# Kernel optimization log

Hardware: AMD Instinct MI355X
Metric: run time of the kernel (lower is better)

## Reference

```python
import jax, jax.numpy as jnp
import numpy as np

B, T, D, H = 2, 2048, 1024, 16
HD = D // H  # head_dim = 64


def apply_rope(x, cos, sin):
    # x: [B, H, T, HD]; cos/sin: [1, 1, T, HD//2]
    x1, x2 = x[..., ::2], x[..., 1::2]
    y1 = x1 * cos - x2 * sin
    y2 = x1 * sin + x2 * cos
    # interleave back: [..., HD//2, 2] -> [..., HD]
    return jnp.stack([y1, y2], axis=-1).reshape(x.shape)


def setup_inputs() -> dict:
    key = jax.random.key(0)
    ks = jax.random.split(key, 11)
    s = 0.02
    return {
        "x": jax.random.normal(ks[0], (B, T, D), jnp.float32),
        "cos": jax.random.normal(ks[1], (1, 1, T, HD // 2), jnp.float32),
        "sin": jax.random.normal(ks[2], (1, 1, T, HD // 2), jnp.float32),
        "Wq": jax.random.normal(ks[3], (D, D), jnp.float32) * s,
        "bq": jax.random.normal(ks[4], (D,), jnp.float32) * s,
        "Wk": jax.random.normal(ks[5], (D, D), jnp.float32) * s,
        "bk": jax.random.normal(ks[6], (D,), jnp.float32) * s,
        "Wv": jax.random.normal(ks[7], (D, D), jnp.float32) * s,
        "bv": jax.random.normal(ks[8], (D,), jnp.float32) * s,
        "Wo": jax.random.normal(ks[9], (D, D), jnp.float32) * s,
        "bo": jax.random.normal(ks[10], (D,), jnp.float32) * s,
    }


def reference(x, cos, sin, Wq, bq, Wk, bk, Wv, bv, Wo, bo):
    b, t, d = x.shape
    # projections (nn.Linear: x @ W.T + b)
    q = (x @ Wq.T + bq).reshape(b, t, H, HD).transpose(0, 2, 1, 3)
    k = (x @ Wk.T + bk).reshape(b, t, H, HD).transpose(0, 2, 1, 3)
    v = (x @ Wv.T + bv).reshape(b, t, H, HD).transpose(0, 2, 1, 3)
    q = apply_rope(q, cos, sin)
    k = apply_rope(k, cos, sin)
    scores = jnp.einsum("bhqd,bhkd->bhqk", q, k) / jnp.sqrt(jnp.asarray(HD, x.dtype))
    # causal mask: query i attends to keys j <= i
    causal = jnp.tril(jnp.ones((t, t), dtype=bool))
    scores = jnp.where(causal, scores, jnp.asarray(-jnp.inf, x.dtype))
    weights = jax.nn.softmax(scores, axis=-1)
    out = jnp.einsum("bhqk,bhkd->bhqd", weights, v)
    out = out.transpose(0, 2, 1, 3).reshape(b, t, d)
    return out @ Wo.T + bo
```

## Files before the change

### kernel.cpp

```cpp
#include <hip/hip_runtime.h>
#include <hip/hip_bf16.h>
#include <cstdint>
#include <cstddef>

typedef __attribute__((ext_vector_type(8))) short bf16x8;
typedef __attribute__((ext_vector_type(4))) float f32x4;
typedef __attribute__((ext_vector_type(16))) float f32x16;

#define SCALE2 0.180336880111112f
#define VSTRIDE 2080

__device__ __forceinline__ unsigned short f2bf(float f) {
    unsigned u = __builtin_bit_cast(unsigned, f);
    unsigned r = (u + 0x7FFFu + ((u >> 16) & 1u)) >> 16;
    return (unsigned short)r;
}

__device__ __forceinline__ void gload16(const unsigned short* g, unsigned short* l) {
    __builtin_amdgcn_global_load_lds(
        (const __attribute__((address_space(1))) unsigned int*)(g),
        (__attribute__((address_space(3))) unsigned int*)(l), 16, 0, 0);
}

__global__ void cvt_all(const float* __restrict__ x,
                        const float* __restrict__ wq, const float* __restrict__ wk,
                        const float* __restrict__ wv, const float* __restrict__ wo,
                        unsigned short* __restrict__ xb,
                        unsigned short* __restrict__ wqb, unsigned short* __restrict__ wkb,
                        unsigned short* __restrict__ wvb, unsigned short* __restrict__ wob)
{
    const int y = blockIdx.y;
    const float* src; unsigned short* dst; int n;
    switch (y) {
        case 0: src = x;  dst = xb;  n = 4194304; break;
        case 1: src = wq; dst = wqb; n = 1048576; break;
        case 2: src = wk; dst = wkb; n = 1048576; break;
        case 3: src = wv; dst = wvb; n = 1048576; break;
        default: src = wo; dst = wob; n = 1048576; break;
    }
    const int i = (blockIdx.x * 256 + threadIdx.x) * 4;
    if (i < n) {
        float4 v = *(const float4*)(src + i);
        ushort4 o;
        o.x = f2bf(v.x); o.y = f2bf(v.y); o.z = f2bf(v.z); o.w = f2bf(v.w);
        *(ushort4*)(dst + i) = o;
    }
}

__global__ __launch_bounds__(256) void gemm_qkv(
    const unsigned short* __restrict__ xb,
    const unsigned short* __restrict__ wqb,
    const unsigned short* __restrict__ wkb,
    const unsigned short* __restrict__ wvb,
    const float* __restrict__ bq, const float* __restrict__ bk, const float* __restrict__ bv,
    const float* __restrict__ cosT, const float* __restrict__ sinT,
    unsigned short* __restrict__ Qb, unsigned short* __restrict__ Kb, unsigned short* __restrict__ Vtg)
{
    const int bid = blockIdx.x;
    const int xcd = bid & 7;
    const int s = bid >> 3;
    const int i4 = xcd >> 1, k2 = xcd & 1;
    const int z = s >> 5;
    const int tt = s & 31;
    const int m0 = (i4 * 8 + (tt >> 2)) * 128;
    const int n0 = (k2 * 4 + (tt & 3)) * 128;

    const unsigned short* wb = (z == 0) ? wqb : ((z == 1) ? wkb : wvb);
    const float* bias = (z == 0) ? bq : ((z == 1) ? bk : bv);
    unsigned short* dst = (z == 0) ? Qb : Kb;

    __shared__ __align__(16) unsigned short Al[128 * 32];
    __shared__ __align__(16) unsigned short Bl[128 * 32];
    __shared__ __align__(16) unsigned short Ct[128 * 136];

    const int tid = threadIdx.x;
    const int lane = tid & 63;
    const int w = tid >> 6;
    const int wr = w >> 1, wc = w & 1;
    const int lr = lane & 15, lg = lane >> 4;
    const int srow = tid >> 2, sseg = tid & 3;
    const int wbase = tid & 192;

    f32x4 acc[4][4] = {};

    for (int k0 = 0; k0 < 1024; k0 += 32) {
        __syncthreads();
#pragma unroll
        for (int p = 0; p < 2; ++p) {
            const int row = srow + p * 64;
            gload16(xb + (size_t)(m0 + row) * 1024 + k0 + sseg * 8, Al + (p * 256 + wbase) * 8);
            gload16(wb + (size_t)(n0 + row) * 1024 + k0 + sseg * 8, Bl + (p * 256 + wbase) * 8);
        }
        __syncthreads();
        bf16x8 af[4], bfr[4];
#pragma unroll
        for (int mt = 0; mt < 4; ++mt)
            af[mt] = *(const bf16x8*)(Al + (wr * 64 + mt * 16 + lr) * 32 + lg * 8);
#pragma unroll
        for (int nt = 0; nt < 4; ++nt)
            bfr[nt] = *(const bf16x8*)(Bl + (wc * 64 + nt * 16 + lr) * 32 + lg * 8);
#pragma unroll
        for (int mt = 0; mt < 4; ++mt)
#pragma unroll
            for (int nt = 0; nt < 4; ++nt)
                acc[mt][nt] = __builtin_amdgcn_mfma_f32_16x16x32_bf16(af[mt], bfr[nt], acc[mt][nt], 0, 0, 0);
    }

#pragma unroll
    for (int mt = 0; mt < 4; ++mt) {
#pragma unroll
        for (int nt = 0; nt < 4; ++nt) {
            const int coln = wc * 64 + nt * 16 + lr;
            const int col = n0 + coln;
            const float bcol = bias[col];
            const int hd = col & 63;
#pragma unroll
            for (int r = 0; r < 4; ++r) {
                const int rowm = wr * 64 + mt * 16 + lg * 4 + r;
                float v = acc[mt][nt][r] + bcol;
                if (z < 2) {
                    float part = __shfl_xor(v, 1);
                    const int ttm = (m0 + rowm) & 2047;
                    const int i = hd >> 1;
                    const float cc = cosT[ttm * 32 + i], ss = sinT[ttm * 32 + i];
                    v = (hd & 1) ? (part * ss + v * cc) : (v * cc - part * ss);
                    if (z == 0) v *= SCALE2;
                    Ct[rowm * 136 + coln] = f2bf(v);
                } else {
                    Ct[coln * 136 + rowm] = f2bf(v);
                }
            }
        }
    }
    __syncthreads();
    if (z < 2) {
#pragma unroll
        for (int p = 0; p < 8; ++p) {
            const int u = p * 256 + tid;
            const int row = u >> 4, seg = u & 15;
            bf16x8 vv = *(const bf16x8*)(Ct + row * 136 + seg * 8);
            const int mrow = m0 + row;
            const int ttm = mrow & 2047, bb = mrow >> 11;
            const int col = n0 + seg * 8;
            const int h = col >> 6, hd = col & 63;
            *(bf16x8*)(dst + ((size_t)(bb * 16 + h) * 2048 + ttm) * 64 + hd) = vv;
        }
    } else {
        const int bb = m0 >> 11;
#pragma unroll
        for (int p = 0; p < 8; ++p) {
            const int u = p * 256 + tid;
            const int vrow = u >> 4, seg = u & 15;
            bf16x8 vv = *(const bf16x8*)(Ct + vrow * 136 + seg * 8);
            const int col = n0 + vrow;
            const int h = col >> 6, hd = col & 63;
            const int ttm = (m0 + seg * 8) & 2047;
            *(bf16x8*)(Vtg + ((size_t)(bb * 16 + h) * 64 + hd) * VSTRIDE + ttm) = vv;
        }
    }
}

__global__ __launch_bounds__(256, 3) void attn_fwd(
    const unsigned short* __restrict__ Qb, const unsigned short* __restrict__ Kb,
    const unsigned short* __restrict__ Vtg, unsigned short* __restrict__ attnb)
{
    __shared__ __align__(16) unsigned char smem[49152];

    const int tid = threadIdx.x, lane = tid & 63, w = tid >> 6;
    const int l31 = lane & 31, lh = lane >> 5;
    const int bid = blockIdx.x;
    const int bh = bid & 31;
    const int pi = bid >> 5;
    const int half = w >> 1;
    const int slice = w & 1;
    const int cH = 63 - pi;
    const int c = half ? pi : cH;
    const int smax = cH >> 1;
    const size_t base = (size_t)bh * 131072;
    const int myq = c * 32 + l31;

    const unsigned short* Kg = Kb + base;
    const unsigned short* Vg = Vtg + (size_t)bh * (64 * VSTRIDE);

    bf16x8 qf[4];
#pragma unroll
    for (int s = 0; s < 4; ++s)
        qf[s] = *(const bf16x8*)(Qb + base + (size_t)myq * 64 + s * 16 + lh * 8);

    f32x16 o0 = {}, o1 = {};
    float sm = 0.f;

#define STAGE(S, B)                                                                   \
    {                                                                                 \
        unsigned short* kb_ = (unsigned short*)(smem + (B) * 16384);                  \
        unsigned short* vb_ = (unsigned short*)(smem + (B) * 16384 + 8192);           \
        _Pragma("unroll")                                                             \
        for (int p = 0; p < 2; ++p) {                                                 \
            const int u = p * 256 + tid;                                              \
            const int row = u >> 3, ss = (u & 7) ^ (row & 7);                         \
            gload16(Kg + (size_t)((S) * 64 + row) * 64 + ss * 8, kb_ + (u & ~63) * 8);\
        }                                                                             \
        _Pragma("unroll")                                                             \
        for (int p = 0; p < 2; ++p) {                                                 \
            const int u = p * 256 + tid;                                              \
            const int row = u >> 3, ss = (u & 7) ^ (row & 7);                         \
            gload16(Vg + (size_t)row * VSTRIDE + (S) * 64 + ss * 8, vb_ + (u & ~63) * 8);\
        }                                                                             \
    }

    STAGE(0, 0);
    STAGE(1, 1);
    int bsel = 0;
    for (int s = 0; s <= smax; ++s) {
        if (s < smax) asm volatile("s_waitcnt vmcnt(4)" ::: "memory");
        else          asm volatile("s_waitcnt vmcnt(0)" ::: "memory");
        __syncthreads();
        if (s + 2 <= smax) {
            int b2 = bsel + 2; if (b2 >= 3) b2 -= 3;
            STAGE(s + 2, b2);
        }
        const int t = 2 * s + slice;
        if (t <= c) {
            const unsigned short* Kc = (const unsigned short*)(smem + bsel * 16384);
            const unsigned short* Vc = Kc + 4096;
            const int kvb = t * 32;
            const int sw = l31 & 7;
            const int roff = slice * 32 + l31;

            bf16x8 kf0 = *(const bf16x8*)(Kc + roff * 64 + ((0 + lh) ^ sw) * 8);
            bf16x8 kf1 = *(const bf16x8*)(Kc + roff * 64 + ((2 + lh) ^ sw) * 8);
            bf16x8 kf2 = *(const bf16x8*)(Kc + roff * 64 + ((4 + lh) ^ sw) * 8);
            bf16x8 kf3 = *(const bf16x8*)(Kc + roff * 64 + ((6 + lh) ^ sw) * 8);

            f32x16 st = {};
            st = __builtin_amdgcn_mfma_f32_32x32x16_bf16(kf0, qf[0], st, 0, 0, 0);
            st = __builtin_amdgcn_mfma_f32_32x32x16_bf16(kf1, qf[1], st, 0, 0, 0);
            st = __builtin_amdgcn_mfma_f32_32x32x16_bf16(kf2, qf[2], st, 0, 0, 0);
            st = __builtin_amdgcn_mfma_f32_32x32x16_bf16(kf3, qf[3], st, 0, 0, 0);

            if (t == c) {
#pragma unroll
                for (int r = 0; r < 16; ++r) {
                    const int kv = kvb + (r & 3) + 8 * (r >> 2) + 4 * lh;
                    st[r] = (kv <= myq) ? st[r] : -1e30f;
                }
            }
#pragma unroll
            for (int r = 0; r < 16; ++r) st[r] = exp2f(st[r]);
            {
                float a0 = st[0] + st[1], a1 = st[2] + st[3];
                float a2 = st[4] + st[5], a3 = st[6] + st[7];
                float a4 = st[8] + st[9], a5 = st[10] + st[11];
                float a6 = st[12] + st[13], a7 = st[14] + st[15];
                sm += ((a0 + a1) + (a2 + a3)) + ((a4 + a5) + (a6 + a7));
            }

            unsigned pw0, pw1, pw2, pw3, pw4, pw5, pw6, pw7;
            {
                unsigned a0, a1, b0, b1;
                asm("v_cvt_pk_bf16_f32 %0, %1, %2" : "=v"(a0) : "v"(st[0]), "v"(st[1]));
                asm("v_cvt_pk_bf16_f32 %0, %1, %2" : "=v"(a1) : "v"(st[2]), "v"(st[3]));
                asm("v_cvt_pk_bf16_f32 %0, %1, %2" : "=v"(b0) : "v"(st[4]), "v"(st[5]));
                asm("v_cvt_pk_bf16_f32 %0, %1, %2" : "=v"(b1) : "v"(st[6]), "v"(st[7]));
                asm("v_permlane32_swap_b32 %0, %1" : "+v"(a0), "+v"(b0));
                asm("v_permlane32_swap_b32 %0, %1" : "+v"(a1), "+v"(b1));
                pw0 = a0; pw1 = a1; pw2 = b0; pw3 = b1;
            }
            {
                unsigned a0, a1, b0, b1;
                asm("v_cvt_pk_bf16_f32 %0, %1, %2" : "=v"(a0) : "v"(st[8]), "v"(st[9]));
                asm("v_cvt_pk_bf16_f32 %0, %1, %2" : "=v"(a1) : "v"(st[10]), "v"(st[11]));
                asm("v_cvt_pk_bf16_f32 %0, %1, %2" : "=v"(b0) : "v"(st[12]), "v"(st[13]));
                asm("v_cvt_pk_bf16_f32 %0, %1, %2" : "=v"(b1) : "v"(st[14]), "v"(st[15]));
                asm("v_permlane32_swap_b32 %0, %1" : "+v"(a0), "+v"(b0));
                asm("v_permlane32_swap_b32 %0, %1" : "+v"(a1), "+v"(b1));
                pw4 = a0; pw5 = a1; pw6 = b0; pw7 = b1;
            }

            const int vs0 = (slice * 4 + lh) ^ sw;
            const int vs1 = (slice * 4 + 2 + lh) ^ sw;
            bf16x8 vf00 = *(const bf16x8*)(Vc + l31 * 64 + vs0 * 8);
            bf16x8 vf01 = *(const bf16x8*)(Vc + l31 * 64 + vs1 * 8);
            bf16x8 vf10 = *(const bf16x8*)(Vc + (32 + l31) * 64 + vs0 * 8);
            bf16x8 vf11 = *(const bf16x8*)(Vc + (32 + l31) * 64 + vs1 * 8);

            uint4 h0 = make_uint4(pw0, pw1, pw2, pw3);
            uint4 h1 = make_uint4(pw4, pw5, pw6, pw7);
            bf16x8 pf0 = __builtin_bit_cast(bf16x8, h0);
            bf16x8 pf1 = __builtin_bit_cast(bf16x8, h1);
            o0 = __builtin_amdgcn_mfma_f32_32x32x16_bf16(vf00, pf0, o0, 0, 0, 0);
            o1 = __builtin_amdgcn_mfma_f32_32x32x16_bf16(vf10, pf0, o1, 0, 0, 0);
            o0 = __builtin_amdgcn_mfma_f32_32x32x16_bf16(vf01, pf1, o0, 0, 0, 0);
            o1 = __builtin_amdgcn_mfma_f32_32x32x16_bf16(vf11, pf1, o1, 0, 0, 0);
        }
        bsel += 1; if (bsel == 3) bsel = 0;
    }

    sm += __shfl_xor(sm, 32);

    float* Om = (float*)smem;
    float* Ms = (float*)(smem + 16384);
    __syncthreads();
    if (slice == 1) {
#pragma unroll
        for (int i = 0; i < 16; ++i) Om[(half * 32 + i) * 64 + lane] = o0[i];
#pragma unroll
        for (int i = 0; i < 16; ++i) Om[(half * 32 + 16 + i) * 64 + lane] = o1[i];
        Ms[half * 64 + lane] = sm;
    }
    __syncthreads();
    if (slice == 0) {
        const float s = sm + Ms[half * 64 + lane];
        const float inv = 1.f / s;
        const int b = bh >> 4, h = bh & 15;
        unsigned short* obase = attnb + ((size_t)(b * 2048 + myq)) * 1024 + h * 64;
#pragma unroll
        for (int g = 0; g < 4; ++g) {
            ushort4 u;
            u.x = f2bf((o0[g * 4 + 0] + Om[(half * 32 + g * 4 + 0) * 64 + lane]) * inv);
            u.y = f2bf((o0[g * 4 + 1] + Om[(half * 32 + g * 4 + 1) * 64 + lane]) * inv);
            u.z = f2bf((o0[g * 4 + 2] + Om[(half * 32 + g * 4 + 2) * 64 + lane]) * inv);
            u.w = f2bf((o0[g * 4 + 3] + Om[(half * 32 + g * 4 + 3) * 64 + lane]) * inv);
            *(ushort4*)(obase + g * 8 + lh * 4) = u;
            ushort4 v;
            v.x = f2bf((o1[g * 4 + 0] + Om[(half * 32 + 16 + g * 4 + 0) * 64 + lane]) * inv);
            v.y = f2bf((o1[g * 4 + 1] + Om[(half * 32 + 16 + g * 4 + 1) * 64 + lane]) * inv);
            v.z = f2bf((o1[g * 4 + 2] + Om[(half * 32 + 16 + g * 4 + 2) * 64 + lane]) * inv);
            v.w = f2bf((o1[g * 4 + 3] + Om[(half * 32 + 16 + g * 4 + 3) * 64 + lane]) * inv);
            *(ushort4*)(obase + 32 + g * 8 + lh * 4) = v;
        }
    }
#undef STAGE
}

__global__ __launch_bounds__(256) void gemm_out(
    const unsigned short* __restrict__ ab,
    const unsigned short* __restrict__ wob,
    const float* __restrict__ bo,
    float* __restrict__ out)
{
    __shared__ __align__(16) unsigned short Al[128 * 32];
    __shared__ __align__(16) unsigned short Bl[64 * 32];

    const int bid = blockIdx.x;
    const int xcd = bid & 7;
    const int s = bid >> 3;
    const int i4 = xcd >> 1, k2 = xcd & 1;
    const int m0 = (i4 * 8 + (s >> 3)) * 128;
    const int n0 = (k2 * 8 + (s & 7)) * 64;

    const int tid = threadIdx.x;
    const int lane = tid & 63;
    const int w = tid >> 6;
    const int lr = lane & 15, lg = lane >> 4;

    f32x4 acc[2][4] = {};

    for (int k0 = 0; k0 < 1024; k0 += 32) {
        __syncthreads();
#pragma unroll
        for (int p = 0; p < 2; ++p) {
            const int u = p * 256 + tid;
            const int row = u >> 2, seg = u & 3;
            gload16(ab + (size_t)(m0 + row) * 1024 + k0 + seg * 8, Al + (u & ~63) * 8);
        }
        {
            const int u = tid;
            const int row = u >> 2, seg = u & 3;
            gload16(wob + (size_t)(n0 + row) * 1024 + k0 + seg * 8, Bl + (u & ~63) * 8);
        }
        __syncthreads();
        bf16x8 af[2], bfr[4];
#pragma unroll
        for (int mt = 0; mt < 2; ++mt)
            af[mt] = *(const bf16x8*)(Al + (w * 32 + mt * 16 + lr) * 32 + lg * 8);
#pragma unroll
        for (int nt = 0; nt < 4; ++nt)
            bfr[nt] = *(const bf16x8*)(Bl + (nt * 16 + lr) * 32 + lg * 8);
#pragma unroll
        for (int mt = 0; mt < 2; ++mt)
#pragma unroll
            for (int nt = 0; nt < 4; ++nt)
                acc[mt][nt] = __builtin_amdgcn_mfma_f32_16x16x32_bf16(af[mt], bfr[nt], acc[mt][nt], 0, 0, 0);
    }

#pragma unroll
    for (int mt = 0; mt < 2; ++mt) {
#pragma unroll
        for (int nt = 0; nt < 4; ++nt) {
            const int col = n0 + nt * 16 + lr;
            const float bcol = bo[col];
#pragma unroll
            for (int r = 0; r < 4; ++r) {
                const int mrow = m0 + w * 32 + mt * 16 + lg * 4 + r;
                out[(size_t)mrow * 1024 + col] = acc[mt][nt][r] + bcol;
            }
        }
    }
}

extern "C" void kernel_launch(void* const* d_in, const int* in_sizes, int n_in,
                              void* d_out, int out_size, void* d_ws, size_t ws_size,
                              hipStream_t stream) {
    const float* x    = (const float*)d_in[0];
    const float* cosT = (const float*)d_in[1];
    const float* sinT = (const float*)d_in[2];
    const float* Wq   = (const float*)d_in[3];
    const float* bq   = (const float*)d_in[4];
    const float* Wk   = (const float*)d_in[5];
    const float* bk   = (const float*)d_in[6];
    const float* Wv   = (const float*)d_in[7];
    const float* bv   = (const float*)d_in[8];
    const float* Wo   = (const float*)d_in[9];
    const float* bo   = (const float*)d_in[10];
    float* out = (float*)d_out;

    char* ws = (char*)d_ws;
    unsigned short* xb    = (unsigned short*)(ws + 0);
    unsigned short* attnb = (unsigned short*)(ws + 0);
    unsigned short* wob   = (unsigned short*)(ws + 8388608);
    unsigned short* wqb   = (unsigned short*)(ws + 10485760);
    unsigned short* wkb   = (unsigned short*)(ws + 12582912);
    unsigned short* wvb   = (unsigned short*)(ws + 14680064);
    unsigned short* Qb    = (unsigned short*)(ws + 16777216);
    unsigned short* Kb    = (unsigned short*)(ws + 25165824);
    unsigned short* Vtg   = (unsigned short*)(ws + 33554432);

    cvt_all<<<dim3(4096, 5), 256, 0, stream>>>(x, Wq, Wk, Wv, Wo, xb, wqb, wkb, wvb, wob);
    gemm_qkv<<<dim3(768), 256, 0, stream>>>(xb, wqb, wkb, wvb, bq, bk, bv,
                                            cosT, sinT, Qb, Kb, Vtg);
    attn_fwd<<<dim3(1024), 256, 0, stream>>>(Qb, Kb, Vtg, attnb);
    gemm_out<<<dim3(512), 256, 0, stream>>>(attnb, wob, bo, out);
}
```

Baseline: 117.7 us.

## Share K/V staging across four query chunks per 512-thread attention block

The attention kernel now launches 512 blocks of 512 threads, each processing four 32-row query chunks (63-g, 47-g, 16+g, g) instead of two. Each K/V tile loaded into shared memory is reused by twice as many query chunks, which halves global K/V traffic per query, and each thread issues one K and one V async load per stage. The tradeoff is fewer resident blocks (launch_bounds 512 with no minimum occupancy), a larger shared reduction region, and imbalance inside a block because chunks of different causal lengths all wait on the longest one's loop.

```diff
diff --git a/kernel.cpp b/kernel.cpp
--- a/kernel.cpp
+++ b/kernel.cpp
@@ -160,7 +160,7 @@
     }
 }
 
-__global__ __launch_bounds__(256, 3) void attn_fwd(
+__global__ __launch_bounds__(512) void attn_fwd(
     const unsigned short* __restrict__ Qb, const unsigned short* __restrict__ Kb,
     const unsigned short* __restrict__ Vtg, unsigned short* __restrict__ attnb)
 {
@@ -170,12 +170,11 @@
     const int l31 = lane & 31, lh = lane >> 5;
     const int bid = blockIdx.x;
     const int bh = bid & 31;
-    const int pi = bid >> 5;
-    const int half = w >> 1;
+    const int g = bid >> 5;
+    const int cidx = w >> 1;
     const int slice = w & 1;
-    const int cH = 63 - pi;
-    const int c = half ? pi : cH;
-    const int smax = cH >> 1;
+    const int c = (cidx == 0) ? (63 - g) : ((cidx == 1) ? (47 - g) : ((cidx == 2) ? (16 + g) : g));
+    const int smax = (63 - g) >> 1;
     const size_t base = (size_t)bh * 131072;
     const int myq = c * 32 + l31;
 
@@ -194,25 +193,16 @@
     {                                                                                 \
         unsigned short* kb_ = (unsigned short*)(smem + (B) * 16384);                  \
         unsigned short* vb_ = (unsigned short*)(smem + (B) * 16384 + 8192);           \
-        _Pragma("unroll")                                                             \
-        for (int p = 0; p < 2; ++p) {                                                 \
-            const int u = p * 256 + tid;                                              \
-            const int row = u >> 3, ss = (u & 7) ^ (row & 7);                         \
-            gload16(Kg + (size_t)((S) * 64 + row) * 64 + ss * 8, kb_ + (u & ~63) * 8);\
-        }                                                                             \
-        _Pragma("unroll")                                                             \
-        for (int p = 0; p < 2; ++p) {                                                 \
-            const int u = p * 256 + tid;                                              \
-            const int row = u >> 3, ss = (u & 7) ^ (row & 7);                         \
-            gload16(Vg + (size_t)row * VSTRIDE + (S) * 64 + ss * 8, vb_ + (u & ~63) * 8);\
-        }                                                                             \
+        const int row = tid >> 3, ss = (tid & 7) ^ (row & 7);                         \
+        gload16(Kg + (size_t)((S) * 64 + row) * 64 + ss * 8, kb_ + (tid & ~63) * 8);  \
+        gload16(Vg + (size_t)row * VSTRIDE + (S) * 64 + ss * 8, vb_ + (tid & ~63) * 8);\
     }
 
     STAGE(0, 0);
     STAGE(1, 1);
     int bsel = 0;
     for (int s = 0; s <= smax; ++s) {
-        if (s < smax) asm volatile("s_waitcnt vmcnt(4)" ::: "memory");
+        if (s < smax) asm volatile("s_waitcnt vmcnt(2)" ::: "memory");
         else          asm volatile("s_waitcnt vmcnt(0)" ::: "memory");
         __syncthreads();
         if (s + 2 <= smax) {
@@ -299,35 +289,35 @@
     sm += __shfl_xor(sm, 32);
 
     float* Om = (float*)smem;
-    float* Ms = (float*)(smem + 16384);
+    float* Ms = (float*)(smem + 32768);
     __syncthreads();
     if (slice == 1) {
 #pragma unroll
-        for (int i = 0; i < 16; ++i) Om[(half * 32 + i) * 64 + lane] = o0[i];
-#pragma unroll
-        for (int i = 0; i < 16; ++i) Om[(half * 32 + 16 + i) * 64 + lane] = o1[i];
-        Ms[half * 64 + lane] = sm;
+        for (int i = 0; i < 16; ++i) Om[(cidx * 32 + i) * 64 + lane] = o0[i];
+#pragma unroll
+        for (int i = 0; i < 16; ++i) Om[(cidx * 32 + 16 + i) * 64 + lane] = o1[i];
+        Ms[cidx * 64 + lane] = sm;
     }
     __syncthreads();
     if (slice == 0) {
-        const float s = sm + Ms[half * 64 + lane];
+        const float s = sm + Ms[cidx * 64 + lane];
         const float inv = 1.f / s;
         const int b = bh >> 4, h = bh & 15;
         unsigned short* obase = attnb + ((size_t)(b * 2048 + myq)) * 1024 + h * 64;
 #pragma unroll
-        for (int g = 0; g < 4; ++g) {
+        for (int gg = 0; gg < 4; ++gg) {
             ushort4 u;
-            u.x = f2bf((o0[g * 4 + 0] + Om[(half * 32 + g * 4 + 0) * 64 + lane]) * inv);
-            u.y = f2bf((o0[g * 4 + 1] + Om[(half * 32 + g * 4 + 1) * 64 + lane]) * inv);
-            u.z = f2bf((o0[g * 4 + 2] + Om[(half * 32 + g * 4 + 2) * 64 + lane]) * inv);
-            u.w = f2bf((o0[g * 4 + 3] + Om[(half * 32 + g * 4 + 3) * 64 + lane]) * inv);
-            *(ushort4*)(obase + g * 8 + lh * 4) = u;
+            u.x = f2bf((o0[gg * 4 + 0] + Om[(cidx * 32 + gg * 4 + 0) * 64 + lane]) * inv);
+            u.y = f2bf((o0[gg * 4 + 1] + Om[(cidx * 32 + gg * 4 + 1) * 64 + lane]) * inv);
+            u.z = f2bf((o0[gg * 4 + 2] + Om[(cidx * 32 + gg * 4 + 2) * 64 + lane]) * inv);
+            u.w = f2bf((o0[gg * 4 + 3] + Om[(cidx * 32 + gg * 4 + 3) * 64 + lane]) * inv);
+            *(ushort4*)(obase + gg * 8 + lh * 4) = u;
             ushort4 v;
-            v.x = f2bf((o1[g * 4 + 0] + Om[(half * 32 + 16 + g * 4 + 0) * 64 + lane]) * inv);
-            v.y = f2bf((o1[g * 4 + 1] + Om[(half * 32 + 16 + g * 4 + 1) * 64 + lane]) * inv);
-            v.z = f2bf((o1[g * 4 + 2] + Om[(half * 32 + 16 + g * 4 + 2) * 64 + lane]) * inv);
-            v.w = f2bf((o1[g * 4 + 3] + Om[(half * 32 + 16 + g * 4 + 3) * 64 + lane]) * inv);
-            *(ushort4*)(obase + 32 + g * 8 + lh * 4) = v;
+            v.x = f2bf((o1[gg * 4 + 0] + Om[(cidx * 32 + 16 + gg * 4 + 0) * 64 + lane]) * inv);
+            v.y = f2bf((o1[gg * 4 + 1] + Om[(cidx * 32 + 16 + gg * 4 + 1) * 64 + lane]) * inv);
+            v.z = f2bf((o1[gg * 4 + 2] + Om[(cidx * 32 + 16 + gg * 4 + 2) * 64 + lane]) * inv);
+            v.w = f2bf((o1[gg * 4 + 3] + Om[(cidx * 32 + 16 + gg * 4 + 3) * 64 + lane]) * inv);
+            *(ushort4*)(obase + 32 + gg * 8 + lh * 4) = v;
         }
     }
 #undef STAGE
@@ -429,6 +419,6 @@
     cvt_all<<<dim3(4096, 5), 256, 0, stream>>>(x, Wq, Wk, Wv, Wo, xb, wqb, wkb, wvb, wob);
     gemm_qkv<<<dim3(768), 256, 0, stream>>>(xb, wqb, wkb, wvb, bq, bk, bv,
                                             cosT, sinT, Qb, Kb, Vtg);
-    attn_fwd<<<dim3(1024), 256, 0, stream>>>(Qb, Kb, Vtg, attnb);
+    attn_fwd<<<dim3(512), 512, 0, stream>>>(Qb, Kb, Vtg, attnb);
     gemm_out<<<dim3(512), 256, 0, stream>>>(attnb, wob, bo, out);
 }
```

New measurement: 111.9 us. 1.05x faster.
